# Optimization experiments

Measured on AMD Instinct MI355X. Metric: run time of the kernel, lower is better.

## Reference

```python
import jax, jax.numpy as jnp
import numpy as np

X_SCALE, X_ZP = 0.03, -66      # int8 quant params (qmin=-128, qmax=127)
Y_SCALE, Y_ZP = 0.025, 160     # uint8 quant params (qmin=0, qmax=255)
M = K = N = 4096


def setup_inputs() -> dict:
    key = jax.random.key(0)
    kx, ky = jax.random.split(key)
    # x holds int8-range values [-128, 127], y holds uint8-range values [0, 255]
    x = jax.random.randint(kx, (M, K), -128, 128, dtype=jnp.int32)
    y = jax.random.randint(ky, (K, N), 0, 256, dtype=jnp.int32)
    return {"x": x, "y": y}


def reference(x, y):
    # dequantize_per_tensor: (q - zero_point) * scale  (values already in [qmin, qmax])
    xf = (x.astype(jnp.float32) - X_ZP) * X_SCALE   # [M, K]
    yf = (y.astype(jnp.float32) - Y_ZP) * Y_SCALE   # [K, N]
    return jnp.matmul(xf, yf)                       # [M, N]
```

## Files before the change

kernel.cpp:

```cpp
#include <hip/hip_runtime.h>
#include <stdint.h>

#define Mdim 4096
#define Kdim 4096
#define Ndim 4096

typedef __attribute__((ext_vector_type(4))) int v4i;
typedef __attribute__((ext_vector_type(16))) int v16i;

__device__ __forceinline__ void gload_lds16(const void* g, void* l) {
  __builtin_amdgcn_global_load_lds(
      (__attribute__((address_space(1))) void*)(uintptr_t)g,
      (__attribute__((address_space(3))) void*)(uint32_t)(uintptr_t)l,
      16, 0, 0);
}

__global__ __launch_bounds__(256) void pack_x_kernel(const int* __restrict__ x,
                                                     char* __restrict__ x8,
                                                     int* __restrict__ rsx) {
  const int row = blockIdx.x;
  const int t = threadIdx.x;
  const int4* src = (const int4*)(x + (size_t)row * Kdim);
  int* dst = (int*)(x8 + (size_t)row * Kdim);
  int sum = 0;
#pragma unroll
  for (int i = 0; i < 4; ++i) {
    int4 v = src[t + 256 * i];
    sum += v.x + v.y + v.z + v.w;
    dst[t + 256 * i] =
        (v.x & 0xff) | ((v.y & 0xff) << 8) | ((v.z & 0xff) << 16) | (v.w << 24);
  }
#pragma unroll
  for (int o = 32; o > 0; o >>= 1) sum += __shfl_down(sum, o, 64);
  __shared__ int red[4];
  if ((t & 63) == 0) red[t >> 6] = sum;
  __syncthreads();
  if (t == 0) rsx[row] = red[0] + red[1] + red[2] + red[3];
}

__global__ __launch_bounds__(256) void pack_yt_kernel(const int* __restrict__ y,
                                                      char* __restrict__ yt,
                                                      int* __restrict__ csy) {
  __shared__ int wt[64 * 17];
  const int t = threadIdx.x;
  const int n0 = blockIdx.x * 64;
  const int k0 = blockIdx.y * 64;
  const int c = t & 15;
  const int r0 = t >> 4;
#pragma unroll
  for (int s = 0; s < 4; ++s) {
    const int r = r0 + s * 16;
    int4 v = *(const int4*)(y + (size_t)(k0 + r) * Ndim + n0 + c * 4);
    v.x -= 128; v.y -= 128; v.z -= 128; v.w -= 128;
    wt[r * 17 + c] =
        (v.x & 0xff) | ((v.y & 0xff) << 8) | ((v.z & 0xff) << 16) | (v.w << 24);
  }
  __syncthreads();
  const int n = t >> 2;
  const int kq = t & 3;
  const int colw = n >> 2;
  const int byi = (n & 3) * 8;
  int outw[4];
  int bsum = 0;
#pragma unroll
  for (int j = 0; j < 4; ++j) {
    int b[4];
#pragma unroll
    for (int jj = 0; jj < 4; ++jj) {
      const int word = wt[(kq * 16 + j * 4 + jj) * 17 + colw];
      b[jj] = (word >> byi) & 0xff;
      bsum += (int)(char)b[jj];
    }
    outw[j] = b[0] | (b[1] << 8) | (b[2] << 16) | (b[3] << 24);
  }
  *(int4*)(yt + (size_t)(n0 + n) * Kdim + k0 + kq * 16) =
      make_int4(outw[0], outw[1], outw[2], outw[3]);
  bsum += __shfl_xor(bsum, 1, 64);
  bsum += __shfl_xor(bsum, 2, 64);
  if (kq == 0) atomicAdd(csy + n0 + n, bsum);
}

__global__ __launch_bounds__(512, 2) void gemm_i8_kernel(
    const char* __restrict__ A, const char* __restrict__ B,
    const int* __restrict__ rsx, const int* __restrict__ csy,
    float* __restrict__ out) {
  __shared__ __align__(16) char lds[4 * 32768];
  const int t = threadIdx.x;
  const int l = t & 63;
  const int w = t >> 6;
  const int warow = w >> 1;
  const int wbcol = w & 1;
  const int bm = blockIdx.y * 256;
  const int bn = blockIdx.x * 256;

  v16i acc[2][4];
#pragma unroll
  for (int i = 0; i < 2; ++i)
#pragma unroll
    for (int j = 0; j < 4; ++j)
#pragma unroll
      for (int q = 0; q < 16; ++q) acc[i][j][q] = 0;

  const int srow = t >> 2;
  const int cswz = ((t & 3) ^ ((t >> 3) & 3)) * 16;
  const char* gA = A + (size_t)(bm + srow) * Kdim + cswz;
  const char* gB = B + (size_t)(bn + srow) * Kdim + cswz;

#define STG4(buf_off, koff)                                                   \
  do {                                                                        \
    _Pragma("unroll") for (int i = 0; i < 2; ++i)                             \
        gload_lds16(gA + (koff) + (size_t)i * 128 * Kdim,                     \
                    lds + (buf_off) + i * 8192 + t * 16);                     \
    _Pragma("unroll") for (int i = 0; i < 2; ++i)                             \
        gload_lds16(gB + (koff) + (size_t)i * 128 * Kdim,                     \
                    lds + (buf_off) + 16384 + i * 8192 + t * 16);             \
  } while (0)

  const int arow = warow * 64 + (l & 31);
  const int brow = wbcol * 128 + (l & 31);
  const int lhalf = l >> 5;
  const int lkey = (l >> 1) & 3;
  const int slot0 = ((0 + lhalf) ^ lkey) * 16;
  const int slot1 = ((2 + lhalf) ^ lkey) * 16;

  v4i fa[2][2][2];
  v4i fb[2][2][4];

#define READF(BK, RBO)                                                        \
  do {                                                                        \
    const char* As_ = lds + (RBO);                                            \
    const char* Bs_ = lds + (RBO) + 16384;                                    \
    _Pragma("unroll") for (int i = 0; i < 2; ++i) {                           \
      fa[BK][0][i] = *(const v4i*)(As_ + (arow + i * 32) * 64 + slot0);       \
      fa[BK][1][i] = *(const v4i*)(As_ + (arow + i * 32) * 64 + slot1);       \
    }                                                                         \
    _Pragma("unroll") for (int j = 0; j < 4; ++j) {                           \
      fb[BK][0][j] = *(const v4i*)(Bs_ + (brow + j * 32) * 64 + slot0);       \
      fb[BK][1][j] = *(const v4i*)(Bs_ + (brow + j * 32) * 64 + slot1);       \
    }                                                                         \
  } while (0)

#define MFMA(a, b, c) __builtin_amdgcn_mfma_i32_32x32x32_i8(a, b, c, 0, 0, 0)
#define SETP(n) __builtin_amdgcn_s_setprio(n)
#define FENCE() __builtin_amdgcn_sched_barrier(0)
#define BAR()                                                                 \
  do {                                                                        \
    asm volatile("" ::: "memory");                                            \
    __builtin_amdgcn_s_barrier();                                             \
    asm volatile("" ::: "memory");                                            \
  } while (0)
#define WAITV(n) asm volatile("s_waitcnt vmcnt(" #n ")" ::: "memory")

#define DOMFMA(BK)                                                            \
  do {                                                                        \
    SETP(1);                                                                  \
    _Pragma("unroll") for (int ks = 0; ks < 2; ++ks)                          \
        _Pragma("unroll") for (int i = 0; i < 2; ++i)                         \
            _Pragma("unroll") for (int j = 0; j < 4; ++j)                     \
                acc[i][j] = MFMA(fa[BK][ks][i], fb[BK][ks][j], acc[i][j]);    \
    SETP(0);                                                                  \
  } while (0)

#define TILEX(RBK, RBO, SBO, SKOFF, MBK)                                      \
  do {                                                                        \
    READF(RBK, RBO);                                                          \
    STG4(SBO, SKOFF);                                                         \
    FENCE();                                                                  \
    DOMFMA(MBK);                                                              \
    WAITV(4);                                                                 \
    BAR();                                                                    \
  } while (0)

  STG4(0, 0);
  STG4(32768, 64);
  STG4(65536, 128);
  WAITV(8);
  BAR();
  READF(0, 0);
  WAITV(4);
  BAR();

#pragma unroll 1
  for (int kt = 0; kt < 60; kt += 4) {
    TILEX(1, 32768, 98304, (kt + 3) * 64, 0);
    TILEX(0, 65536, 0, (kt + 4) * 64, 1);
    TILEX(1, 98304, 32768, (kt + 5) * 64, 0);
    TILEX(0, 0, 65536, (kt + 6) * 64, 1);
  }
  TILEX(1, 32768, 98304, 63 * 64, 0);
  READF(0, 65536);
  FENCE();
  DOMFMA(1);
  WAITV(0);
  BAR();
  READF(1, 98304);
  FENCE();
  DOMFMA(0);
  DOMFMA(1);

  const int col = l & 31;
#pragma unroll
  for (int i = 0; i < 2; ++i) {
    const int gm0 = bm + warow * 64 + i * 32;
#pragma unroll
    for (int j = 0; j < 4; ++j) {
      const int gn = bn + wbcol * 128 + j * 32 + col;
      const int cs = 66 * csy[gn] - 8650752;
#pragma unroll
      for (int r = 0; r < 16; ++r) {
        const int row = (r & 3) + 8 * (r >> 2) + 4 * lhalf;
        const int gm = gm0 + row;
        const int val = acc[i][j][r] - 32 * rsx[gm] + cs;
        out[(size_t)gm * Ndim + gn] = 7.5e-4f * (float)val;
      }
    }
  }
#undef STG4
#undef READF
#undef TILEX
#undef DOMFMA
#undef MFMA
#undef SETP
#undef FENCE
#undef BAR
#undef WAITV
}

extern "C" void kernel_launch(void* const* d_in, const int* in_sizes, int n_in,
                              void* d_out, int out_size, void* d_ws, size_t ws_size,
                              hipStream_t stream) {
  (void)in_sizes; (void)n_in; (void)out_size; (void)ws_size;
  const int* x = (const int*)d_in[0];
  const int* y = (const int*)d_in[1];
  float* out = (float*)d_out;
  char* ws = (char*)d_ws;
  char* x8 = ws;
  char* yt = ws + (size_t)Mdim * Kdim;
  int* rsx = (int*)(ws + (size_t)Mdim * Kdim + (size_t)Kdim * Ndim);
  int* csy = rsx + Mdim;

  hipMemsetAsync(csy, 0, Ndim * sizeof(int), stream);
  pack_x_kernel<<<Mdim, 256, 0, stream>>>(x, x8, rsx);
  pack_yt_kernel<<<dim3(Ndim / 64, Kdim / 64), 256, 0, stream>>>(y, yt, csy);
  gemm_i8_kernel<<<dim3(Ndim / 256, Mdim / 256), 512, 0, stream>>>(x8, yt, rsx, csy, out);
}
```

Measured before the change: 242.3 us.

## Pre-pack B into MFMA fragment order and load it directly into registers

```diff
diff --git a/kernel.cpp b/kernel.cpp
--- a/kernel.cpp
+++ b/kernel.cpp
@@ -73,8 +73,16 @@
     }
     outw[j] = b[0] | (b[1] << 8) | (b[2] << 16) | (b[3] << 24);
   }
-  *(int4*)(yt + (size_t)(n0 + n) * Kdim + k0 + kq * 16) =
-      make_int4(outw[0], outw[1], outw[2], outw[3]);
+  {
+    const int n_abs = n0 + n;
+    const int k_abs = k0 + kq * 16;
+    const int nblk = n_abs >> 5;
+    const int lane16 = ((k_abs >> 4) & 1) * 32 + (n_abs & 31);
+    const int kt_ = k_abs >> 6;
+    const int ks_ = (k_abs >> 5) & 1;
+    *(int4*)(yt + (size_t)nblk * 131072 + kt_ * 2048 + ks_ * 1024 +
+             lane16 * 16) = make_int4(outw[0], outw[1], outw[2], outw[3]);
+  }
   bsum += __shfl_xor(bsum, 1, 64);
   bsum += __shfl_xor(bsum, 2, 64);
   if (kq == 0) atomicAdd(csy + n0 + n, bsum);
@@ -84,14 +92,19 @@
     const char* __restrict__ A, const char* __restrict__ B,
     const int* __restrict__ rsx, const int* __restrict__ csy,
     float* __restrict__ out) {
-  __shared__ __align__(16) char lds[4 * 32768];
+  __shared__ __align__(16) char lds[4 * 16384];
   const int t = threadIdx.x;
   const int l = t & 63;
   const int w = t >> 6;
   const int warow = w >> 1;
   const int wbcol = w & 1;
-  const int bm = blockIdx.y * 256;
-  const int bn = blockIdx.x * 256;
+  const int d = blockIdx.y * 16 + blockIdx.x;
+  const int q = d >> 3;
+  const int xcd = d & 7;
+  const int bnid = xcd * 2 + (q >> 4);
+  const int bmid = q & 15;
+  const int bm = bmid * 256;
+  const int bn = bnid * 256;
 
   v16i acc[2][4];
 #pragma unroll
@@ -99,50 +112,50 @@
 #pragma unroll
     for (int j = 0; j < 4; ++j)
 #pragma unroll
-      for (int q = 0; q < 16; ++q) acc[i][j][q] = 0;
+      for (int q2 = 0; q2 < 16; ++q2) acc[i][j][q2] = 0;
 
   const int srow = t >> 2;
   const int cswz = ((t & 3) ^ ((t >> 3) & 3)) * 16;
   const char* gA = A + (size_t)(bm + srow) * Kdim + cswz;
-  const char* gB = B + (size_t)(bn + srow) * Kdim + cswz;
-
-#define STG4(buf_off, koff)                                                   \
+
+#define STG_A(buf_off, koff)                                                  \
   do {                                                                        \
     _Pragma("unroll") for (int i = 0; i < 2; ++i)                             \
         gload_lds16(gA + (koff) + (size_t)i * 128 * Kdim,                     \
                     lds + (buf_off) + i * 8192 + t * 16);                     \
-    _Pragma("unroll") for (int i = 0; i < 2; ++i)                             \
-        gload_lds16(gB + (koff) + (size_t)i * 128 * Kdim,                     \
-                    lds + (buf_off) + 16384 + i * 8192 + t * 16);             \
   } while (0)
 
   const int arow = warow * 64 + (l & 31);
-  const int brow = wbcol * 128 + (l & 31);
   const int lhalf = l >> 5;
   const int lkey = (l >> 1) & 3;
   const int slot0 = ((0 + lhalf) ^ lkey) * 16;
   const int slot1 = ((2 + lhalf) ^ lkey) * 16;
 
+  const char* gBf =
+      B + (size_t)(bnid * 8 + wbcol * 4) * 131072 + (size_t)l * 16;
+
   v4i fa[2][2][2];
   v4i fb[2][2][4];
 
-#define READF(BK, RBO)                                                        \
+#define READF_A(BK, RBO)                                                      \
   do {                                                                        \
     const char* As_ = lds + (RBO);                                            \
-    const char* Bs_ = lds + (RBO) + 16384;                                    \
     _Pragma("unroll") for (int i = 0; i < 2; ++i) {                           \
       fa[BK][0][i] = *(const v4i*)(As_ + (arow + i * 32) * 64 + slot0);       \
       fa[BK][1][i] = *(const v4i*)(As_ + (arow + i * 32) * 64 + slot1);       \
     }                                                                         \
-    _Pragma("unroll") for (int j = 0; j < 4; ++j) {                           \
-      fb[BK][0][j] = *(const v4i*)(Bs_ + (brow + j * 32) * 64 + slot0);       \
-      fb[BK][1][j] = *(const v4i*)(Bs_ + (brow + j * 32) * 64 + slot1);       \
-    }                                                                         \
+  } while (0)
+
+#define READ_B(BK, kt_)                                                       \
+  do {                                                                        \
+    _Pragma("unroll") for (int j = 0; j < 4; ++j)                             \
+        _Pragma("unroll") for (int ks = 0; ks < 2; ++ks)                      \
+            fb[BK][ks][j] = *(const v4i*)(gBf + (size_t)j * 131072 +          \
+                                          (size_t)(kt_)*2048 + ks * 1024);    \
   } while (0)
 
 #define MFMA(a, b, c) __builtin_amdgcn_mfma_i32_32x32x32_i8(a, b, c, 0, 0, 0)
 #define SETP(n) __builtin_amdgcn_s_setprio(n)
-#define FENCE() __builtin_amdgcn_sched_barrier(0)
 #define BAR()                                                                 \
   do {                                                                        \
     asm volatile("" ::: "memory");                                            \
@@ -161,41 +174,43 @@
     SETP(0);                                                                  \
   } while (0)
 
-#define TILEX(RBK, RBO, SBO, SKOFF, MBK)                                      \
-  do {                                                                        \
-    READF(RBK, RBO);                                                          \
-    STG4(SBO, SKOFF);                                                         \
-    FENCE();                                                                  \
-    DOMFMA(MBK);                                                              \
-    WAITV(4);                                                                 \
+#define TILE(LBK, RBO, SBO, SKOFF, KB, CBK)                                   \
+  do {                                                                        \
+    READF_A(LBK, RBO);                                                        \
+    READ_B(LBK, KB);                                                          \
+    STG_A(SBO, SKOFF);                                                        \
+    WAITV(10);                                                                \
+    DOMFMA(CBK);                                                              \
     BAR();                                                                    \
   } while (0)
 
-  STG4(0, 0);
-  STG4(32768, 64);
-  STG4(65536, 128);
+  STG_A(0, 0);
+  STG_A(16384, 64);
+  STG_A(32768, 128);
+  __builtin_amdgcn_sched_barrier(0);
+  READ_B(0, 0);
   WAITV(8);
   BAR();
-  READF(0, 0);
-  WAITV(4);
-  BAR();
+  READF_A(0, 0);
 
 #pragma unroll 1
   for (int kt = 0; kt < 60; kt += 4) {
-    TILEX(1, 32768, 98304, (kt + 3) * 64, 0);
-    TILEX(0, 65536, 0, (kt + 4) * 64, 1);
-    TILEX(1, 98304, 32768, (kt + 5) * 64, 0);
-    TILEX(0, 0, 65536, (kt + 6) * 64, 1);
-  }
-  TILEX(1, 32768, 98304, 63 * 64, 0);
-  READF(0, 65536);
-  FENCE();
+    TILE(1, 16384, 49152, (kt + 3) * 64, kt + 1, 0);
+    TILE(0, 32768, 0, (kt + 4) * 64, kt + 2, 1);
+    TILE(1, 49152, 16384, (kt + 5) * 64, kt + 3, 0);
+    TILE(0, 0, 32768, (kt + 6) * 64, kt + 4, 1);
+  }
+  TILE(1, 16384, 49152, 63 * 64, 61, 0);
+  READF_A(0, 32768);
+  READ_B(0, 62);
+  WAITV(8);
   DOMFMA(1);
+  BAR();
+  READF_A(1, 49152);
+  READ_B(1, 63);
+  WAITV(8);
+  DOMFMA(0);
   WAITV(0);
-  BAR();
-  READF(1, 98304);
-  FENCE();
-  DOMFMA(0);
   DOMFMA(1);
 
   const int col = l & 31;
@@ -215,13 +230,13 @@
       }
     }
   }
-#undef STG4
-#undef READF
-#undef TILEX
+#undef STG_A
+#undef READF_A
+#undef READ_B
+#undef TILE
 #undef DOMFMA
 #undef MFMA
 #undef SETP
-#undef FENCE
 #undef BAR
 #undef WAITV
 }
```

Result: slower. 248.6 us (+2.6%).
